# Optimization experiments

Measured on AMD Instinct MI355X. Metric: run time of the kernel, lower is better.

The kernel has to match this reference:

```python
import jax, jax.numpy as jnp
import numpy as np

MAX_DISP = 200


def conv2d(x, w, b):
    # x: [N,C,H,W], w: [O,I,3,3], stride 1, pad 1 == SAME
    y = jax.lax.conv_general_dilated(x, w, (1, 1), 'SAME',
                                     dimension_numbers=('NCHW', 'OIHW', 'NCHW'))
    return y + b[None, :, None, None]


def bn(x, g, b, m, v):
    # eval-mode BatchNorm2d with running stats (eps=1e-5)
    inv = jax.lax.rsqrt(v[None, :, None, None] + 1e-5)
    return g[None, :, None, None] * (x - m[None, :, None, None]) * inv + b[None, :, None, None]


def cost_volume(left, right, max_disp):
    # left, right: [c,h,w]. cost[d,y,x] = sum_c left[c,y,x] * padded[c,y,x+d]
    # where padded = [zeros(c,h,D), right] along w -- exact math of the torch loop.
    c, h, w = left.shape
    padded = jnp.concatenate([jnp.zeros((c, h, max_disp), left.dtype), right], axis=-1)

    def corr(d):
        win = jax.lax.dynamic_slice_in_dim(padded, d, w, axis=2)  # [c,h,w]
        return jnp.sum(left * win, axis=0)  # [h,w]

    return jax.vmap(corr)(jnp.arange(max_disp))  # [D,h,w]


def setup_inputs() -> dict:
    key = jax.random.key(0)
    ks = jax.random.split(key, 32)
    C, H, W = 32, 128, 256
    D = MAX_DISP
    inp = {}
    inp['left'] = jax.random.normal(ks[0], (1, C, H, W), jnp.float32)
    inp['right'] = jax.random.normal(ks[1], (1, C, H, W), jnp.float32)
    chans = [(64, D), (32, 64), (8, 32)]
    i = 2
    for idx, (co, ci) in enumerate(chans, 1):
        inp[f'w{idx}'] = jax.random.normal(ks[i], (co, ci, 3, 3), jnp.float32) * 0.05; i += 1
        inp[f'b{idx}'] = jax.random.normal(ks[i], (co,), jnp.float32) * 0.05; i += 1
        inp[f'g{idx}'] = 1.0 + 0.1 * jax.random.normal(ks[i], (co,), jnp.float32); i += 1
        inp[f'be{idx}'] = 0.1 * jax.random.normal(ks[i], (co,), jnp.float32); i += 1
        inp[f'm{idx}'] = 0.1 * jax.random.normal(ks[i], (co,), jnp.float32); i += 1
        inp[f'v{idx}'] = jax.random.uniform(ks[i], (co,), jnp.float32, minval=0.5, maxval=1.5); i += 1
    inp['w4'] = jax.random.normal(ks[i], (1, 8, 3, 3), jnp.float32) * 0.05; i += 1
    inp['b4'] = jax.random.normal(ks[i], (1,), jnp.float32) * 0.05
    return inp


def reference(left, right, w1, b1, g1, be1, m1, v1, w2, b2, g2, be2, m2, v2,
              w3, b3, g3, be3, m3, v3, w4, b4):
    vol = cost_volume(left[0], right[0], MAX_DISP)[None]  # [1, D, H, W]
    x = jax.nn.relu(bn(conv2d(vol, w1, b1), g1, be1, m1, v1))
    x = jax.nn.relu(bn(conv2d(x, w2, b2), g2, be2, m2, v2))
    x = jax.nn.relu(bn(conv2d(x, w3, b3), g3, be3, m3, v3))
    x = conv2d(x, w4, b4)
    return x[0]  # [1, H, W] (torch squeezes batch dim 0)
```

## Files before the change

kernel.cpp:

```cpp
#include <hip/hip_runtime.h>

#define HH 128
#define WW 256
#define CV_C 32
#define DISP 200

typedef __attribute__((ext_vector_type(4))) float f32x4;
typedef __attribute__((ext_vector_type(8))) short bf16x8;

__device__ inline unsigned short f2bf(float f) {
  unsigned int u = __float_as_uint(f);
  u = (u + 0x7FFFu + ((u >> 16) & 1u)) >> 16;
  return (unsigned short)u;
}

__device__ inline float bf2f(short s) {
  return __uint_as_float(((unsigned int)(unsigned short)s) << 16);
}

#define MAP_YX4()                                   \
  const int slot = bid >> 3;                        \
  const int y = ((bid & 7) << 4) + (slot & 15);     \
  const int x0 = (slot >> 4) << 6;

__global__ __launch_bounds__(256) void k1_cv_pack(
    const float* __restrict__ left, const float* __restrict__ right,
    const float* __restrict__ w1, const float* __restrict__ w2,
    const float* __restrict__ w3, unsigned short* __restrict__ pw1,
    unsigned short* __restrict__ pb2, unsigned short* __restrict__ pb3,
    unsigned short* __restrict__ cost_t) {
  __shared__ unsigned short r_sh[272][40];
  __shared__ unsigned short l_hi[64][40];
  __shared__ unsigned short l_lo[64][40];
  __shared__ unsigned short c_sh[64][224];
  const int bid = blockIdx.x;
  const int tid = threadIdx.x;

  if (bid >= 512) {
    const int b = bid - 512;
    if (b < 504) {
      const int idx = b * 256 + tid;
      const int j = idx & 7;
      const int n = (idx >> 3) & 63;
      const int kg = (idx >> 9) & 3;
      const int cp = idx >> 11;
      const int pos = cp % 9;
      const int chunk = cp / 9;
      const int ci = chunk * 32 + kg * 8 + j;
      float v = 0.f;
      if (ci < 200) v = w1[(n * 200 + ci) * 9 + pos];
      pw1[idx] = f2bf(v);
    } else if (b < 576) {
      const int idx = (b - 504) * 256 + tid;
      const int j = idx & 7;
      const int n = (idx >> 3) & 31;
      const int kg = (idx >> 8) & 3;
      const int kc = (idx >> 10) & 1;
      const int pos = idx >> 11;
      const int ci = kc * 32 + kg * 8 + j;
      pb2[idx] = f2bf(w2[(n * 64 + ci) * 9 + pos]);
    } else {
      const int idx = (b - 576) * 256 + tid;
      const int j = idx & 7;
      const int n = (idx >> 3) & 15;
      const int kg = (idx >> 7) & 3;
      const int pos = idx >> 9;
      const int ci = kg * 8 + j;
      float v = 0.f;
      if (n < 8) v = w3[(n * 32 + ci) * 9 + pos];
      pb3[idx] = f2bf(v);
    }
    return;
  }

  MAP_YX4();
  const int lane = tid & 63;
  const int wv = tid >> 6;
  const int col = lane & 15;
  const int kg = lane >> 4;

  for (int c = wv; c < CV_C; c += 4) {
    const float v = left[(c * HH + y) * WW + x0 + lane];
    const unsigned short h = f2bf(v);
    l_hi[lane][c] = h;
    l_lo[lane][c] = f2bf(v - bf2f(h));
  }
  for (int c = wv; c < CV_C; c += 4) {
    for (int pq = 0; pq < 320; pq += 64) {
      const int p = pq + lane;
      if (p < 272) {
        const int xp = x0 - 208 + p;
        float v = (xp >= 0) ? right[(c * HH + y) * WW + xp] : 0.f;
        r_sh[p][c] = f2bf(v);
      }
    }
  }
  {
    bf16x8 z = {0, 0, 0, 0, 0, 0, 0, 0};
    bf16x8* cz = (bf16x8*)c_sh;
#pragma unroll
    for (int k = 0; k < 7; ++k) cz[k * 256 + tid] = z;
  }
  __syncthreads();

  const bf16x8 b_hi = *(const bf16x8*)&l_hi[16 * wv + col][kg * 8];
  const bf16x8 b_lo = *(const bf16x8*)&l_lo[16 * wv + col][kg * 8];

  for (int t = 0; t < 14; ++t) {
    const int pq = 16 * (wv - t) + 208;
    const bf16x8 a_r = *(const bf16x8*)&r_sh[pq + col][kg * 8];
    f32x4 acc = {0.f, 0.f, 0.f, 0.f};
    acc = __builtin_amdgcn_mfma_f32_16x16x32_bf16(a_r, b_hi, acc, 0, 0, 0);
    acc = __builtin_amdgcn_mfma_f32_16x16x32_bf16(a_r, b_lo, acc, 0, 0, 0);
#pragma unroll
    for (int r = 0; r < 4; ++r) {
      const int d = 200 - 16 * t + kg * 4 + r - col;
      if (d >= 0 && d < DISP) c_sh[16 * wv + col][d] = f2bf(acc[r]);
    }
  }
  __syncthreads();

#pragma unroll
  for (int k = 0; k < 7; ++k) {
    const int s = k * 256 + tid;
    const int x = s / 28;
    const int dv = s - x * 28;
    *reinterpret_cast<bf16x8*>(&cost_t[(y * WW + x0 + x) * 224 + dv * 8]) =
        *reinterpret_cast<const bf16x8*>(&c_sh[x][dv * 8]);
  }
}

__global__ __launch_bounds__(256) void conv1_mfma_kernel(
    const unsigned short* __restrict__ cost_t,
    const unsigned short* __restrict__ pw,
    const float* __restrict__ bias, const float* __restrict__ gam,
    const float* __restrict__ bet, const float* __restrict__ mean,
    const float* __restrict__ var, unsigned short* __restrict__ out_t) {
  __shared__ unsigned short a_sh[3 * 66 * 40];
  __shared__ unsigned short b_sh[9 * 4 * 64 * 8];
  const int bid = blockIdx.x;
  const int tid = threadIdx.x;
  MAP_YX4();
  const int lane = tid & 63;
  const int wv = tid >> 6;
  const int m0 = (wv >> 1) * 32;
  const int n0 = (wv & 1) * 32;
  const int col = lane & 15;
  const int kg = lane >> 4;

  long goff[4];
  int laddr[4];
  bool gvalid[4], lvalid[4];
#pragma unroll
  for (int it = 0; it < 4; ++it) {
    const int i = tid + it * 256;
    lvalid[it] = i < 792;
    const int row = i / 264;
    const int rem = i % 264;
    const int xx = rem >> 2;
    const int q = rem & 3;
    const int gy = y + row - 1;
    const int gx = x0 - 1 + xx;
    gvalid[it] = lvalid[it] && gy >= 0 && gy < HH && gx >= 0 && gx < WW;
    goff[it] = gvalid[it] ? (long)(gy * WW + gx) * 224 + q * 8 : 0;
    laddr[it] = (row * 66 + xx) * 40 + q * 8;
  }

  f32x4 acc[2][2];
#pragma unroll
  for (int i = 0; i < 2; ++i)
#pragma unroll
    for (int jx = 0; jx < 2; ++jx) acc[i][jx] = 0.f;

  const bf16x8* pwv = (const bf16x8*)pw;
  bf16x8* bsl = (bf16x8*)b_sh;
  const bf16x8 zero = {0, 0, 0, 0, 0, 0, 0, 0};
  bf16x8 stgA[4], stgB[9];

#pragma unroll
  for (int it = 0; it < 4; ++it)
    stgA[it] = gvalid[it] ? *reinterpret_cast<const bf16x8*>(&cost_t[goff[it]])
                          : zero;
#pragma unroll
  for (int it = 0; it < 9; ++it) stgB[it] = pwv[tid + it * 256];
#pragma unroll
  for (int it = 0; it < 4; ++it)
    if (lvalid[it]) *reinterpret_cast<bf16x8*>(&a_sh[laddr[it]]) = stgA[it];
#pragma unroll
  for (int it = 0; it < 9; ++it) bsl[tid + it * 256] = stgB[it];
  __syncthreads();

  for (int chunk = 0; chunk < 7; ++chunk) {
    if (chunk < 6) {
#pragma unroll
      for (int it = 0; it < 4; ++it)
        stgA[it] = gvalid[it] ? *reinterpret_cast<const bf16x8*>(
                                    &cost_t[goff[it] + (chunk + 1) * 32])
                              : zero;
      const bf16x8* pwn = pwv + (chunk + 1) * 2304;
#pragma unroll
      for (int it = 0; it < 9; ++it) stgB[it] = pwn[tid + it * 256];
    }
    const bf16x8* av = (const bf16x8*)a_sh;
#pragma unroll
    for (int pos = 0; pos < 9; ++pos) {
      const int ky = pos / 3;
      const int kx = pos % 3;
      const bf16x8 b0v = bsl[(pos * 4 + kg) * 64 + n0 + col];
      const bf16x8 b1v = bsl[(pos * 4 + kg) * 64 + n0 + 16 + col];
      const bf16x8 a0v = av[(ky * 66 + m0 + col + kx) * 5 + kg];
      const bf16x8 a1v = av[(ky * 66 + m0 + 16 + col + kx) * 5 + kg];
      acc[0][0] = __builtin_amdgcn_mfma_f32_16x16x32_bf16(a0v, b0v, acc[0][0], 0, 0, 0);
      acc[0][1] = __builtin_amdgcn_mfma_f32_16x16x32_bf16(a0v, b1v, acc[0][1], 0, 0, 0);
      acc[1][0] = __builtin_amdgcn_mfma_f32_16x16x32_bf16(a1v, b0v, acc[1][0], 0, 0, 0);
      acc[1][1] = __builtin_amdgcn_mfma_f32_16x16x32_bf16(a1v, b1v, acc[1][1], 0, 0, 0);
    }
    if (chunk < 6) {
      __syncthreads();
#pragma unroll
      for (int it = 0; it < 4; ++it)
        if (lvalid[it]) *reinterpret_cast<bf16x8*>(&a_sh[laddr[it]]) = stgA[it];
#pragma unroll
      for (int it = 0; it < 9; ++it) bsl[tid + it * 256] = stgB[it];
      __syncthreads();
    }
  }

#pragma unroll
  for (int nf = 0; nf < 2; ++nf) {
    const int c = n0 + nf * 16 + col;
    const float inv = rsqrtf(var[c] + 1e-5f);
    const float sc = gam[c] * inv;
    const float sh = bet[c] - mean[c] * sc;
    const float bb = bias[c];
#pragma unroll
    for (int mf = 0; mf < 2; ++mf) {
#pragma unroll
      for (int rr = 0; rr < 4; ++rr) {
        const int m = m0 + mf * 16 + kg * 4 + rr;
        float vv = (acc[mf][nf][rr] + bb) * sc + sh;
        vv = fmaxf(vv, 0.f);
        out_t[((y * WW + x0 + m) << 6) + c] = f2bf(vv);
      }
    }
  }
}

__global__ __launch_bounds__(256) void conv2_mfma_kernel(
    const unsigned short* __restrict__ in_t,
    const unsigned short* __restrict__ pb,
    const float* __restrict__ bias, const float* __restrict__ gam,
    const float* __restrict__ bet, const float* __restrict__ mean,
    const float* __restrict__ var, unsigned short* __restrict__ out_t) {
  __shared__ unsigned short a_sh[3 * 66 * 64];
  __shared__ unsigned short b_sh[18432];
  char* const ab = (char*)a_sh;
  const int bid = blockIdx.x;
  const int tid = threadIdx.x;
  MAP_YX4();
  const int lane = tid & 63;
  const int wv = tid >> 6;
  const int m0 = (wv >> 1) * 32;
  const int n0 = (wv & 1) * 16;
  const int col = lane & 15;
  const int kg = lane >> 4;

  f32x4 acc[2];
  acc[0] = 0.f;
  acc[1] = 0.f;

  {
    const bf16x8* pbv = (const bf16x8*)pb;
    bf16x8* bsl = (bf16x8*)b_sh;
#pragma unroll
    for (int it = 0; it < 9; ++it) bsl[tid + it * 256] = pbv[tid + it * 256];
  }
  for (int i = tid; i < 1584; i += 256) {
    const int r = i >> 3;
    const int q = i & 7;
    const int rowy = r / 66;
    const int xx = r % 66;
    const int gy = y + rowy - 1;
    const int gx = x0 - 1 + xx;
    bf16x8 v = {0, 0, 0, 0, 0, 0, 0, 0};
    if (gy >= 0 && gy < HH && gx >= 0 && gx < WW)
      v = *reinterpret_cast<const bf16x8*>(&in_t[((gy * WW + gx) << 6) + q * 8]);
    const int byte = ((r << 7) + (q << 4)) ^ ((r & 7) << 4);
    *reinterpret_cast<bf16x8*>(ab + byte) = v;
  }
  __syncthreads();

  const bf16x8* bsl = (const bf16x8*)b_sh;
#pragma unroll
  for (int pos = 0; pos < 9; ++pos) {
    const int ky = pos / 3;
    const int kx = pos % 3;
#pragma unroll
    for (int kc = 0; kc < 2; ++kc) {
      const bf16x8 bv = bsl[((pos * 2 + kc) * 4 + kg) * 32 + n0 + col];
#pragma unroll
      for (int mf = 0; mf < 2; ++mf) {
        const int r = ky * 66 + m0 + mf * 16 + col + kx;
        const int byte = ((r << 7) + (kc << 6) + (kg << 4)) ^ ((r & 7) << 4);
        const bf16x8 av = *reinterpret_cast<const bf16x8*>(ab + byte);
        acc[mf] = __builtin_amdgcn_mfma_f32_16x16x32_bf16(av, bv, acc[mf], 0, 0, 0);
      }
    }
  }

  const int c = n0 + col;
  const float inv = rsqrtf(var[c] + 1e-5f);
  const float sc = gam[c] * inv;
  const float sh = bet[c] - mean[c] * sc;
  const float bb = bias[c];
#pragma unroll
  for (int mf = 0; mf < 2; ++mf) {
#pragma unroll
    for (int rr = 0; rr < 4; ++rr) {
      const int m = m0 + mf * 16 + kg * 4 + rr;
      float vv = (acc[mf][rr] + bb) * sc + sh;
      vv = fmaxf(vv, 0.f);
      out_t[((y * WW + x0 + m) << 5) + c] = f2bf(vv);
    }
  }
}

__global__ __launch_bounds__(256) void conv3_mfma_kernel(
    const unsigned short* __restrict__ in_t,
    const unsigned short* __restrict__ pb,
    const float* __restrict__ bias, const float* __restrict__ gam,
    const float* __restrict__ bet, const float* __restrict__ mean,
    const float* __restrict__ var, unsigned short* __restrict__ out_t) {
  __shared__ unsigned short a_sh[3 * 66 * 32];
  __shared__ unsigned short b_sh[4608];
  char* const ab = (char*)a_sh;
  const int bid = blockIdx.x;
  const int tid = threadIdx.x;
  MAP_YX4();
  const int lane = tid & 63;
  const int wv = tid >> 6;
  const int m0 = wv * 16;
  const int col = lane & 15;
  const int kg = lane >> 4;

  f32x4 acc = 0.f;

  {
    const bf16x8* pbv = (const bf16x8*)pb;
    bf16x8* bsl = (bf16x8*)b_sh;
    for (int s = tid; s < 576; s += 256) bsl[s] = pbv[s];
  }
  for (int i = tid; i < 792; i += 256) {
    const int r = i >> 2;
    const int q = i & 3;
    const int rowy = r / 66;
    const int xx = r % 66;
    const int gy = y + rowy - 1;
    const int gx = x0 - 1 + xx;
    bf16x8 v = {0, 0, 0, 0, 0, 0, 0, 0};
    if (gy >= 0 && gy < HH && gx >= 0 && gx < WW)
      v = *reinterpret_cast<const bf16x8*>(&in_t[((gy * WW + gx) << 5) + q * 8]);
    const int byte = ((r << 6) + (q << 4)) ^ ((r & 3) << 4);
    *reinterpret_cast<bf16x8*>(ab + byte) = v;
  }
  __syncthreads();

  const bf16x8* bsl = (const bf16x8*)b_sh;
#pragma unroll
  for (int pos = 0; pos < 9; ++pos) {
    const int ky = pos / 3;
    const int kx = pos % 3;
    const bf16x8 bv = bsl[(pos * 4 + kg) * 16 + col];
    const int r = ky * 66 + m0 + col + kx;
    const int byte = ((r << 6) + (kg << 4)) ^ ((r & 3) << 4);
    const bf16x8 av = *reinterpret_cast<const bf16x8*>(ab + byte);
    acc = __builtin_amdgcn_mfma_f32_16x16x32_bf16(av, bv, acc, 0, 0, 0);
  }

  if (col < 8) {
    const int c = col;
    const float inv = rsqrtf(var[c] + 1e-5f);
    const float sc = gam[c] * inv;
    const float sh = bet[c] - mean[c] * sc;
    const float bb = bias[c];
#pragma unroll
    for (int rr = 0; rr < 4; ++rr) {
      const int m = m0 + kg * 4 + rr;
      float vv = (acc[rr] + bb) * sc + sh;
      vv = fmaxf(vv, 0.f);
      out_t[((y * WW + x0 + m) << 3) + c] = f2bf(vv);
    }
  }
}

__global__ __launch_bounds__(256) void conv4_kernel(
    const unsigned short* __restrict__ in_t, const float* __restrict__ w4,
    const float* __restrict__ b4, float* __restrict__ out) {
  const int bid = blockIdx.x;
  const int y = ((bid & 7) << 4) + (bid >> 3);
  const int x = threadIdx.x;

  float wr[3][3][8];
#pragma unroll
  for (int ci = 0; ci < 8; ++ci)
#pragma unroll
    for (int ky = 0; ky < 3; ++ky)
#pragma unroll
      for (int kx = 0; kx < 3; ++kx) wr[ky][kx][ci] = w4[(ci * 3 + ky) * 3 + kx];

  float acc = b4[0];
#pragma unroll
  for (int ky = 0; ky < 3; ++ky) {
    const int gy = y + ky - 1;
    if (gy < 0 || gy >= HH) continue;
#pragma unroll
    for (int kx = 0; kx < 3; ++kx) {
      const int gx = x + kx - 1;
      if (gx < 0 || gx >= WW) continue;
      const bf16x8 v =
          *reinterpret_cast<const bf16x8*>(&in_t[((gy << 8) + gx) << 3]);
#pragma unroll
      for (int ci = 0; ci < 8; ++ci) acc += bf2f(v[ci]) * wr[ky][kx][ci];
    }
  }
  out[y * WW + x] = acc;
}

extern "C" void kernel_launch(void* const* d_in, const int* in_sizes, int n_in,
                              void* d_out, int out_size, void* d_ws,
                              size_t ws_size, hipStream_t stream) {
  const float* left = (const float*)d_in[0];
  const float* right = (const float*)d_in[1];
  const float* w1 = (const float*)d_in[2];
  const float* b1 = (const float*)d_in[3];
  const float* g1 = (const float*)d_in[4];
  const float* be1 = (const float*)d_in[5];
  const float* m1 = (const float*)d_in[6];
  const float* v1 = (const float*)d_in[7];
  const float* w2 = (const float*)d_in[8];
  const float* b2 = (const float*)d_in[9];
  const float* g2 = (const float*)d_in[10];
  const float* be2 = (const float*)d_in[11];
  const float* m2 = (const float*)d_in[12];
  const float* v2 = (const float*)d_in[13];
  const float* w3 = (const float*)d_in[14];
  const float* b3 = (const float*)d_in[15];
  const float* g3 = (const float*)d_in[16];
  const float* be3 = (const float*)d_in[17];
  const float* m3 = (const float*)d_in[18];
  const float* v3 = (const float*)d_in[19];
  const float* w4 = (const float*)d_in[20];
  const float* b4 = (const float*)d_in[21];

  char* ws = (char*)d_ws;
  unsigned short* cost_t = (unsigned short*)ws;
  char* region = ws + 14680064;
  unsigned short* pw1 = (unsigned short*)(region + 0);
  unsigned short* pb2 = (unsigned short*)(region + 262144);
  unsigned short* pb3 = (unsigned short*)(region + 327680);
  unsigned short* o1t = (unsigned short*)(region + 393216);
  unsigned short* o2t = (unsigned short*)(region + 4587520);
  unsigned short* o3t = (unsigned short*)(region + 6684672);
  float* o4 = (float*)d_out;

  k1_cv_pack<<<1106, 256, 0, stream>>>(left, right, w1, w2, w3, pw1, pb2, pb3,
                                       cost_t);
  conv1_mfma_kernel<<<512, 256, 0, stream>>>(cost_t, pw1, b1, g1, be1, m1, v1,
                                             o1t);
  conv2_mfma_kernel<<<512, 256, 0, stream>>>(o1t, pb2, b2, g2, be2, m2, v2,
                                             o2t);
  conv3_mfma_kernel<<<512, 256, 0, stream>>>(o2t, pb3, b3, g3, be3, m3, v3,
                                             o3t);
  conv4_kernel<<<128, 256, 0, stream>>>(o3t, w4, b4, o4);
}
```

Measured before the change: 49.29 us.

## Compute two output rows per block in conv1 to reuse halo and weights

conv1 now handles a 2-row by 64-column output tile per block, staging 4 input rows instead of 3 and loading the weight chunk once for twice the outputs. Each wave computes one row with 4 M-tiles by 2 N-tiles of MFMA, and the grid is halved to 256 blocks. This cuts redundant halo-row and weight traffic per output. In exchange it uses more LDS and accumulator registers, and with only 256 blocks the GPU may not be fully occupied.

```diff
diff --git a/kernel.cpp b/kernel.cpp
--- a/kernel.cpp
+++ b/kernel.cpp
@@ -136,55 +136,58 @@
     const float* __restrict__ bias, const float* __restrict__ gam,
     const float* __restrict__ bet, const float* __restrict__ mean,
     const float* __restrict__ var, unsigned short* __restrict__ out_t) {
-  __shared__ unsigned short a_sh[3 * 66 * 40];
+  __shared__ unsigned short a_sh[4 * 66 * 40];
   __shared__ unsigned short b_sh[9 * 4 * 64 * 8];
   const int bid = blockIdx.x;
   const int tid = threadIdx.x;
-  MAP_YX4();
+  const int slot = bid >> 3;
+  const int p = ((bid & 7) << 3) + (slot & 7);
+  const int y0 = p << 1;
+  const int x0 = (slot >> 3) << 6;
   const int lane = tid & 63;
   const int wv = tid >> 6;
-  const int m0 = (wv >> 1) * 32;
+  const int r = wv >> 1;
   const int n0 = (wv & 1) * 32;
   const int col = lane & 15;
   const int kg = lane >> 4;
 
-  long goff[4];
-  int laddr[4];
-  bool gvalid[4], lvalid[4];
-#pragma unroll
-  for (int it = 0; it < 4; ++it) {
+  long goff[5];
+  int laddr[5];
+  bool gvalid[5], lvalid[5];
+#pragma unroll
+  for (int it = 0; it < 5; ++it) {
     const int i = tid + it * 256;
-    lvalid[it] = i < 792;
+    lvalid[it] = i < 1056;
     const int row = i / 264;
     const int rem = i % 264;
     const int xx = rem >> 2;
     const int q = rem & 3;
-    const int gy = y + row - 1;
+    const int gy = y0 + row - 1;
     const int gx = x0 - 1 + xx;
     gvalid[it] = lvalid[it] && gy >= 0 && gy < HH && gx >= 0 && gx < WW;
     goff[it] = gvalid[it] ? (long)(gy * WW + gx) * 224 + q * 8 : 0;
     laddr[it] = (row * 66 + xx) * 40 + q * 8;
   }
 
-  f32x4 acc[2][2];
-#pragma unroll
-  for (int i = 0; i < 2; ++i)
+  f32x4 acc[4][2];
+#pragma unroll
+  for (int i = 0; i < 4; ++i)
 #pragma unroll
     for (int jx = 0; jx < 2; ++jx) acc[i][jx] = 0.f;
 
   const bf16x8* pwv = (const bf16x8*)pw;
   bf16x8* bsl = (bf16x8*)b_sh;
   const bf16x8 zero = {0, 0, 0, 0, 0, 0, 0, 0};
-  bf16x8 stgA[4], stgB[9];
-
-#pragma unroll
-  for (int it = 0; it < 4; ++it)
+  bf16x8 stgA[5], stgB[9];
+
+#pragma unroll
+  for (int it = 0; it < 5; ++it)
     stgA[it] = gvalid[it] ? *reinterpret_cast<const bf16x8*>(&cost_t[goff[it]])
                           : zero;
 #pragma unroll
   for (int it = 0; it < 9; ++it) stgB[it] = pwv[tid + it * 256];
 #pragma unroll
-  for (int it = 0; it < 4; ++it)
+  for (int it = 0; it < 5; ++it)
     if (lvalid[it]) *reinterpret_cast<bf16x8*>(&a_sh[laddr[it]]) = stgA[it];
 #pragma unroll
   for (int it = 0; it < 9; ++it) bsl[tid + it * 256] = stgB[it];
@@ -193,7 +196,7 @@
   for (int chunk = 0; chunk < 7; ++chunk) {
     if (chunk < 6) {
 #pragma unroll
-      for (int it = 0; it < 4; ++it)
+      for (int it = 0; it < 5; ++it)
         stgA[it] = gvalid[it] ? *reinterpret_cast<const bf16x8*>(
                                     &cost_t[goff[it] + (chunk + 1) * 32])
                               : zero;
@@ -208,17 +211,22 @@
       const int kx = pos % 3;
       const bf16x8 b0v = bsl[(pos * 4 + kg) * 64 + n0 + col];
       const bf16x8 b1v = bsl[(pos * 4 + kg) * 64 + n0 + 16 + col];
-      const bf16x8 a0v = av[(ky * 66 + m0 + col + kx) * 5 + kg];
-      const bf16x8 a1v = av[(ky * 66 + m0 + 16 + col + kx) * 5 + kg];
-      acc[0][0] = __builtin_amdgcn_mfma_f32_16x16x32_bf16(a0v, b0v, acc[0][0], 0, 0, 0);
-      acc[0][1] = __builtin_amdgcn_mfma_f32_16x16x32_bf16(a0v, b1v, acc[0][1], 0, 0, 0);
-      acc[1][0] = __builtin_amdgcn_mfma_f32_16x16x32_bf16(a1v, b0v, acc[1][0], 0, 0, 0);
-      acc[1][1] = __builtin_amdgcn_mfma_f32_16x16x32_bf16(a1v, b1v, acc[1][1], 0, 0, 0);
+      bf16x8 af[4];
+#pragma unroll
+      for (int mt = 0; mt < 4; ++mt)
+        af[mt] = av[((r + ky) * 66 + mt * 16 + col + kx) * 5 + kg];
+#pragma unroll
+      for (int mt = 0; mt < 4; ++mt) {
+        acc[mt][0] =
+            __builtin_amdgcn_mfma_f32_16x16x32_bf16(af[mt], b0v, acc[mt][0], 0, 0, 0);
+        acc[mt][1] =
+            __builtin_amdgcn_mfma_f32_16x16x32_bf16(af[mt], b1v, acc[mt][1], 0, 0, 0);
+      }
     }
     if (chunk < 6) {
       __syncthreads();
 #pragma unroll
-      for (int it = 0; it < 4; ++it)
+      for (int it = 0; it < 5; ++it)
         if (lvalid[it]) *reinterpret_cast<bf16x8*>(&a_sh[laddr[it]]) = stgA[it];
 #pragma unroll
       for (int it = 0; it < 9; ++it) bsl[tid + it * 256] = stgB[it];
@@ -226,6 +234,7 @@
     }
   }
 
+  const int y = y0 + r;
 #pragma unroll
   for (int nf = 0; nf < 2; ++nf) {
     const int c = n0 + nf * 16 + col;
@@ -234,11 +243,11 @@
     const float sh = bet[c] - mean[c] * sc;
     const float bb = bias[c];
 #pragma unroll
-    for (int mf = 0; mf < 2; ++mf) {
+    for (int mt = 0; mt < 4; ++mt) {
 #pragma unroll
       for (int rr = 0; rr < 4; ++rr) {
-        const int m = m0 + mf * 16 + kg * 4 + rr;
-        float vv = (acc[mf][nf][rr] + bb) * sc + sh;
+        const int m = mt * 16 + kg * 4 + rr;
+        float vv = (acc[mt][nf][rr] + bb) * sc + sh;
         vv = fmaxf(vv, 0.f);
         out_t[((y * WW + x0 + m) << 6) + c] = f2bf(vv);
       }
@@ -465,7 +474,7 @@
 
   k1_cv_pack<<<1106, 256, 0, stream>>>(left, right, w1, w2, w3, pw1, pb2, pb3,
                                        cost_t);
-  conv1_mfma_kernel<<<512, 256, 0, stream>>>(cost_t, pw1, b1, g1, be1, m1, v1,
+  conv1_mfma_kernel<<<256, 256, 0, stream>>>(cost_t, pw1, b1, g1, be1, m1, v1,
                                              o1t);
   conv2_mfma_kernel<<<512, 256, 0, stream>>>(o1t, pb2, b2, g2, be2, m2, v2,
                                              o2t);
```

Result: no change. 48.88 us (-0.8%).
